# Performance work log

Hardware: AMD Instinct MI355X
Metric: run time of the kernel (lower is better)

The kernel has to match this reference:

```python
import jax, jax.numpy as jnp
import numpy as np

N, D, C = 8192, 512, 16
HM, HG = 256, 64  # mlp hidden, gcn hidden
ENHANCE = 6.0
LW0, LW1 = 1.0, 1.0  # loss_weight
NEG = jnp.float32(-9e15)


def setup_inputs() -> dict:
    key = jax.random.key(0)
    ks = jax.random.split(key, 12)
    feature = jax.random.normal(ks[0], (N, D), dtype=jnp.float32)
    # sparse symmetric binary adjacency with self loops (avg degree ~ 65)
    A = (jax.random.uniform(ks[1], (N, N)) < 0.004).astype(jnp.float32)
    adj = jnp.maximum(jnp.maximum(A, A.T), jnp.eye(N, dtype=jnp.float32))
    node_labels = jax.random.randint(ks[2], (N,), 0, C)
    labels_oneHot = jax.nn.one_hot(node_labels, C, dtype=jnp.float32)
    bias = jnp.ones((C, C), jnp.float32) + (ENHANCE - 1.0) * jnp.eye(C, dtype=jnp.float32)
    s = 0.05
    Wm1 = s * jax.random.normal(ks[3], (D, HM), dtype=jnp.float32)
    bm1 = jnp.zeros((HM,), jnp.float32)
    Wm2 = s * jax.random.normal(ks[4], (HM, C), dtype=jnp.float32)
    bm2 = jnp.zeros((C,), jnp.float32)
    W1 = s * jax.random.normal(ks[5], (D, HG), dtype=jnp.float32)
    b1 = jnp.zeros((HG,), jnp.float32)
    W2 = s * jax.random.normal(ks[6], (HG, C), dtype=jnp.float32)
    b2 = jnp.zeros((C,), jnp.float32)
    idx = jax.random.randint(ks[7], (1024,), 0, N)
    label = node_labels[idx]
    mask = jax.random.randint(ks[8], (N,), 0, 2).astype(bool)  # train mask
    return {"feature": feature, "adj": adj, "labels_oneHot": labels_oneHot,
            "bias": bias, "Wm1": Wm1, "bm1": bm1, "Wm2": Wm2, "bm2": bm2,
            "W1": W1, "b1": b1, "W2": W2, "b2": b2,
            "idx": idx, "label": label, "mask": mask}


def reference(feature, adj, labels_oneHot, bias, Wm1, bm1, Wm2, bm2,
              W1, b1, W2, b2, idx, label, mask):
    # MLP soft labels B: [N, C]
    B = jax.nn.softmax(jnp.maximum(feature @ Wm1 + bm1, 0.0) @ Wm2 + bm2, axis=1)
    # block matrix H: ground truth labels on train nodes, soft labels elsewhere
    soft_y = jnp.where(mask[:, None], labels_oneHot, B)          # [N, C]
    Hm = soft_y.T @ adj                                          # [C, N]
    H = (Hm @ soft_y) / jnp.sum(Hm, axis=1, keepdims=True)       # [C, C]
    Q = (H @ H.T) * bias
    Q = Q / jnp.sum(Q, axis=1, keepdims=True)                    # [C, C]
    # edge score B Q B^T, adjacency-masked softmax
    score = (B @ Q @ B.T) * adj                                  # [N, N]
    g = jax.nn.softmax(jnp.where(adj > 0, score, NEG), axis=1)   # [N, N]
    # 2-layer GCN with g as propagation matrix
    h = jnp.maximum(g @ (feature @ W1) + b1, 0.0)                # [N, HG]
    output = g @ (h @ W2) + b2                                   # [N, C]
    logits = jax.nn.softmax(output, axis=1)
    gcn_loss = -jnp.mean(jnp.log(logits[idx, label]))
    mlp_loss = -jnp.mean(jnp.log(B[idx, label]))
    final_loss = LW0 * gcn_loss + LW1 * mlp_loss
    return logits, final_loss, jax.lax.stop_gradient(H), jax.lax.stop_gradient(Q), jax.lax.stop_gradient(output)
```

## Files before the change

### kernel.cpp

```cpp
#include <hip/hip_runtime.h>
#include <math.h>

#define N   8192
#define D   512
#define C   16
#define HM  256
#define HG  64
#define KMAX 128

typedef __attribute__((ext_vector_type(8))) short bf16x8;
typedef __attribute__((ext_vector_type(4))) float f32x4;
typedef unsigned long long ull;

__device__ __forceinline__ unsigned short f2b(float x) {
  union { float f; unsigned int u; } v; v.f = x;
  unsigned int r = v.u + 0x7FFFu + ((v.u >> 16) & 1u);
  return (unsigned short)(r >> 16);
}
__device__ __forceinline__ float b2f(unsigned short b) {
  union { unsigned int u; float f; } v; v.u = ((unsigned int)b) << 16;
  return v.f;
}

__global__ __launch_bounds__(256) void tile_ballot(const float* __restrict__ adj,
    ull* __restrict__ bm, const float* __restrict__ Wm1, const float* __restrict__ W1,
    const float* __restrict__ Wm2, unsigned short* __restrict__ Wt,
    unsigned short* __restrict__ Wm2tb) {
  const int t = threadIdx.x;
  if (blockIdx.y == 64) {
    const int start = blockIdx.x * 256 + t;
    for (int i = start; i < 320 * 512; i += 129 * 256) {
      const int n = i >> 9, k = i & 511;
      Wt[i] = f2b((n < 256) ? Wm1[k * 256 + n] : W1[k * 64 + (n - 256)]);
    }
    for (int i = start; i < 16 * 256; i += 129 * 256) {
      const int cc = i >> 8, k = i & 255;
      Wm2tb[i] = f2b(Wm2[k * 16 + cc]);
    }
    return;
  }
  const int p = blockIdx.y;
  int I, J;
  if ((int)blockIdx.x < 128 - p) { I = p; J = p + blockIdx.x; }
  else                           { I = 127 - p; J = blockIdx.x - 1; }
  __shared__ unsigned char tb[64][68];
  #pragma unroll
  for (int rr = 0; rr < 4; ++rr) {
    const int r = rr * 16 + (t >> 4);
    const int c = (t & 15) * 4;
    const float4 v = *(const float4*)&adj[(size_t)(I * 64 + r) * N + J * 64 + c];
    tb[r][c + 0] = v.x > 0.f;
    tb[r][c + 1] = v.y > 0.f;
    tb[r][c + 2] = v.z > 0.f;
    tb[r][c + 3] = v.w > 0.f;
  }
  __syncthreads();
  const int lane = t & 63, w = t >> 6;
  #pragma unroll
  for (int i = 0; i < 16; ++i) {
    const int r = w * 16 + i;
    const ull rw = __ballot(tb[r][lane] != 0);
    if (lane == 0) bm[(size_t)(I * 64 + r) * 128 + J] = rw;
    const ull cw = __ballot(tb[lane][r] != 0);
    if (lane == 0) bm[(size_t)(J * 64 + r) * 128 + I] = cw;
  }
}

__global__ __launch_bounds__(256) void gemm_mlp(
    const float* __restrict__ feature, const bf16x8* __restrict__ Wt,
    const float* __restrict__ bm1, const bf16x8* __restrict__ Wm2tb,
    const float* __restrict__ bm2, const float* __restrict__ labels1h,
    const int* __restrict__ mask, float* __restrict__ Bmat,
    float* __restrict__ softy, unsigned short* __restrict__ X1b) {
  __shared__ unsigned short c1[32][264];
  const int l = threadIdx.x & 63, w = threadIdx.x >> 6;
  const int m0 = blockIdx.x * 32;
  const int kb = l >> 4, cl = l & 15;
  const int rw = (w >> 1) * 16;
  const int nt0 = (w & 1) * 10;
  const int row = m0 + rw + cl;
  const float* arow = feature + (size_t)row * D + kb * 8;
  f32x4 acc[10] = {};
  for (int kk = 0; kk < 16; ++kk) {
    const float4 a0 = *(const float4*)&arow[kk * 32];
    const float4 a1 = *(const float4*)&arow[kk * 32 + 4];
    bf16x8 af;
    af[0] = f2b(a0.x); af[1] = f2b(a0.y); af[2] = f2b(a0.z); af[3] = f2b(a0.w);
    af[4] = f2b(a1.x); af[5] = f2b(a1.y); af[6] = f2b(a1.z); af[7] = f2b(a1.w);
    #pragma unroll
    for (int i = 0; i < 10; ++i) {
      const bf16x8 bfr = Wt[(size_t)((nt0 + i) * 16 + cl) * 64 + kk * 4 + kb];
      acc[i] = __builtin_amdgcn_mfma_f32_16x16x32_bf16(af, bfr, acc[i], 0, 0, 0);
    }
  }
  const int rl0 = rw + kb * 4;
  #pragma unroll
  for (int i = 0; i < 10; ++i) {
    const int nt = nt0 + i;
    const int col = nt * 16 + cl;
    if (nt < 16) {
      const float bv = bm1[col];
      #pragma unroll
      for (int r = 0; r < 4; ++r)
        c1[rl0 + r][col] = f2b(fmaxf(acc[i][r] + bv, 0.f));
    } else {
      const int xc = col - 256;
      #pragma unroll
      for (int r = 0; r < 4; ++r)
        X1b[(size_t)(m0 + rl0 + r) * HG + xc] = f2b(acc[i][r]);
    }
  }
  __syncthreads();
  if ((w & 1) == 0) {
    f32x4 acc2 = {0.f, 0.f, 0.f, 0.f};
    #pragma unroll
    for (int kk = 0; kk < 8; ++kk) {
      const bf16x8 a2 = *(const bf16x8*)&c1[rw + cl][kk * 32 + kb * 8];
      const bf16x8 b2v = Wm2tb[(size_t)cl * 32 + kk * 4 + kb];
      acc2 = __builtin_amdgcn_mfma_f32_16x16x32_bf16(a2, b2v, acc2, 0, 0, 0);
    }
    const float bm2v = bm2[cl];
    #pragma unroll
    for (int r = 0; r < 4; ++r) {
      float v = acc2[r] + bm2v;
      float m = v;
      #pragma unroll
      for (int s = 1; s < 16; s <<= 1) m = fmaxf(m, __shfl_xor(m, s));
      const float e = __expf(v - m);
      float ssum = e;
      #pragma unroll
      for (int s = 1; s < 16; s <<= 1) ssum += __shfl_xor(ssum, s);
      const float bb = e / ssum;
      const int grow = m0 + rw + kb * 4 + r;
      Bmat[grow * C + cl] = bb;
      softy[grow * C + cl] = mask[grow] ? labels1h[grow * C + cl] : bb;
    }
  }
}

__global__ __launch_bounds__(256) void extract_nbr(const ull* __restrict__ bm,
    int* __restrict__ rowcnt, int* __restrict__ colidx,
    const float* __restrict__ softy, float* __restrict__ nbrsum) {
  __shared__ int cs[4][128];
  const int t = threadIdx.x, lane = t & 63, w = t >> 6;
  const int row = blockIdx.x * 4 + w;
  const ull w0 = bm[(size_t)row * 128 + lane];
  const ull w1 = bm[(size_t)row * 128 + 64 + lane];
  const int c0 = __builtin_popcountll(w0);
  const int c1 = __builtin_popcountll(w1);
  int s0 = c0, s1 = c1;
  #pragma unroll
  for (int s = 1; s < 64; s <<= 1) {
    const int y0 = __shfl_up(s0, s);
    const int y1 = __shfl_up(s1, s);
    if (lane >= s) { s0 += y0; s1 += y1; }
  }
  const int total0 = __shfl(s0, 63);
  const int total = total0 + __shfl(s1, 63);
  int off = s0 - c0;
  ull x = w0;
  while (x) {
    const int b = __builtin_ctzll(x);
    if (off < KMAX) {
      const int col = lane * 64 + b;
      colidx[(size_t)row * KMAX + off] = col;
      cs[w][off] = col;
    }
    ++off;
    x &= x - 1;
  }
  off = total0 + s1 - c1;
  x = w1;
  while (x) {
    const int b = __builtin_ctzll(x);
    if (off < KMAX) {
      const int col = (64 + lane) * 64 + b;
      colidx[(size_t)row * KMAX + off] = col;
      cs[w][off] = col;
    }
    ++off;
    x &= x - 1;
  }
  const int cnt = min(total, KMAX);
  if (lane == 0) rowcnt[row] = cnt;
  __syncthreads();
  const int cc = lane & 15, grp = lane >> 4;
  float acc = 0.f;
  for (int e = grp; e < cnt; e += 4)
    acc += softy[cs[w][e] * C + cc];
  acc += __shfl_xor(acc, 16);
  acc += __shfl_xor(acc, 32);
  if (lane < 16) nbrsum[row * C + cc] = acc;
}

__global__ __launch_bounds__(256) void h_partial(const float* __restrict__ nbrsum,
    const float* __restrict__ softy, float* __restrict__ Hpart) {
  const int t = threadIdx.x;
  const int c = t >> 4, cp = t & 15;
  float acc = 0.f, dacc = 0.f;
  const int j0 = blockIdx.x * (N / 64);
  for (int j = j0; j < j0 + N / 64; ++j) {
    const float nv = nbrsum[j * C + c];
    acc = fmaf(nv, softy[j * C + cp], acc);
    if (cp == 0) dacc += nv;
  }
  Hpart[blockIdx.x * 272 + t] = acc;
  if (cp == 0) Hpart[blockIdx.x * 272 + 256 + c] = dacc;
}

__global__ __launch_bounds__(256) void hq_final(const float* __restrict__ Hpart,
    const float* __restrict__ bias, float* __restrict__ H_out,
    float* __restrict__ Q_out, float* __restrict__ Qws) {
  __shared__ float Hs[256], Qs[256], rs[16], dd[16];
  const int t = threadIdx.x;
  const int c = t >> 4, cp = t & 15;
  float acc = 0.f;
  for (int b = 0; b < 64; ++b) acc += Hpart[b * 272 + t];
  if (t < 16) {
    float s = 0.f;
    for (int b = 0; b < 64; ++b) s += Hpart[b * 272 + 256 + t];
    dd[t] = s;
  }
  __syncthreads();
  const float Hv = acc / dd[c];
  Hs[t] = Hv;
  H_out[t] = Hv;
  __syncthreads();
  float q = 0.f;
  for (int k = 0; k < 16; ++k) q = fmaf(Hs[c * 16 + k], Hs[cp * 16 + k], q);
  q *= bias[t];
  Qs[t] = q;
  __syncthreads();
  if (t < 16) {
    float s = 0.f;
    for (int k = 0; k < 16; ++k) s += Qs[t * 16 + k];
    rs[t] = s;
  }
  __syncthreads();
  const float Qv = q / rs[c];
  Q_out[t] = Qv;
  Qws[t] = Qv;
}

__global__ __launch_bounds__(256) void edge_gcn1(const float* __restrict__ Bmat,
    const float* __restrict__ Q, const int* __restrict__ rowcnt,
    const int* __restrict__ colidx, const unsigned short* __restrict__ X1b,
    const float* __restrict__ b1, const float* __restrict__ W2,
    float* __restrict__ gval, float* __restrict__ X2) {
  __shared__ float Prow[4][16];
  __shared__ float gv[4][128];
  __shared__ int cs[4][128];
  const int lane = threadIdx.x & 63, w = threadIdx.x >> 6;
  const int row = blockIdx.x * 4 + w;
  const int c = lane & 15, grp = lane >> 4;
  float acc = 0.f;
  for (int k = grp * 4; k < grp * 4 + 4; ++k)
    acc = fmaf(Bmat[row * C + k], Q[k * C + c], acc);
  acc += __shfl_xor(acc, 16);
  acc += __shfl_xor(acc, 32);
  if (lane < 16) Prow[w][c] = acc;
  __syncthreads();
  const int cnt = rowcnt[row];
  const int col0 = (lane < cnt) ? colidx[row * KMAX + lane] : 0;
  const int col1 = (lane + 64 < cnt) ? colidx[row * KMAX + lane + 64] : 0;
  float s0 = -1e30f, s1 = -1e30f;
  if (lane < cnt) {
    float s = 0.f;
    for (int k = 0; k < 16; ++k) s = fmaf(Prow[w][k], Bmat[col0 * C + k], s);
    s0 = s;
  }
  if (lane + 64 < cnt) {
    float s = 0.f;
    for (int k = 0; k < 16; ++k) s = fmaf(Prow[w][k], Bmat[col1 * C + k], s);
    s1 = s;
  }
  float m = fmaxf(s0, s1);
  for (int s = 1; s < 64; s <<= 1) m = fmaxf(m, __shfl_xor(m, s));
  const float e0 = __expf(s0 - m), e1 = __expf(s1 - m);
  float ssum = e0 + e1;
  for (int s = 1; s < 64; s <<= 1) ssum += __shfl_xor(ssum, s);
  const float inv = 1.f / ssum;
  const float g0 = e0 * inv, g1 = e1 * inv;
  if (lane < cnt) gval[row * KMAX + lane] = g0;
  if (lane + 64 < cnt) gval[row * KMAX + lane + 64] = g1;
  gv[w][lane] = g0; gv[w][lane + 64] = g1;
  cs[w][lane] = col0; cs[w][lane + 64] = col1;
  __syncthreads();
  float hacc = 0.f;
  for (int e = 0; e < cnt; ++e)
    hacc = fmaf(gv[w][e], b2f(X1b[(size_t)cs[w][e] * HG + lane]), hacc);
  const float h = fmaxf(hacc + b1[lane], 0.f);
  float x[16];
  #pragma unroll
  for (int cc = 0; cc < 16; ++cc) x[cc] = h * W2[lane * C + cc];
  #pragma unroll
  for (int s = 1; s < 64; s <<= 1)
    #pragma unroll
    for (int cc = 0; cc < 16; ++cc) x[cc] += __shfl_xor(x[cc], s);
  float v = x[0];
  #pragma unroll
  for (int cc = 1; cc < 16; ++cc) v = (lane == cc) ? x[cc] : v;
  if (lane < 16) X2[row * C + lane] = v;
}

__global__ __launch_bounds__(256) void gcn2(const float* __restrict__ X2,
    const float* __restrict__ b2, const int* __restrict__ rowcnt,
    const int* __restrict__ colidx, const float* __restrict__ gval,
    float* __restrict__ out_logits, float* __restrict__ out_output) {
  const int lane = threadIdx.x & 63;
  const int row = blockIdx.x * 4 + (threadIdx.x >> 6);
  const int c = lane & 15, grp = lane >> 4;
  const int cnt = rowcnt[row];
  float acc = 0.f;
  for (int e = grp; e < cnt; e += 4)
    acc = fmaf(gval[row * KMAX + e], X2[colidx[row * KMAX + e] * C + c], acc);
  acc += __shfl_xor(acc, 16);
  acc += __shfl_xor(acc, 32);
  acc += b2[c];
  float m = acc;
  for (int s = 1; s < 16; s <<= 1) m = fmaxf(m, __shfl_xor(m, s));
  const float e = __expf(acc - m);
  float ssum = e;
  for (int s = 1; s < 16; s <<= 1) ssum += __shfl_xor(ssum, s);
  if (lane < 16) {
    out_output[row * C + c] = acc;
    out_logits[row * C + c] = e / ssum;
  }
}

__global__ __launch_bounds__(256) void loss_kernel(const float* __restrict__ logits,
    const float* __restrict__ Bmat, const int* __restrict__ idx,
    const int* __restrict__ label, float* __restrict__ out_loss) {
  __shared__ float sg[256], sm[256];
  const int t = threadIdx.x;
  float g = 0.f, m = 0.f;
  for (int i = t; i < 1024; i += 256) {
    const int ii = idx[i], ll = label[i];
    g -= logf(logits[ii * C + ll]);
    m -= logf(Bmat[ii * C + ll]);
  }
  sg[t] = g; sm[t] = m;
  __syncthreads();
  for (int s = 128; s > 0; s >>= 1) {
    if (t < s) { sg[t] += sg[t + s]; sm[t] += sm[t + s]; }
    __syncthreads();
  }
  if (t == 0) out_loss[0] = 1.0f * (sg[0] / 1024.f) + 1.0f * (sm[0] / 1024.f);
}

extern "C" void kernel_launch(void* const* d_in, const int* in_sizes, int n_in,
                              void* d_out, int out_size, void* d_ws, size_t ws_size,
                              hipStream_t stream) {
  const float* feature  = (const float*)d_in[0];
  const float* adj      = (const float*)d_in[1];
  const float* labels1h = (const float*)d_in[2];
  const float* bias     = (const float*)d_in[3];
  const float* Wm1 = (const float*)d_in[4];
  const float* bm1 = (const float*)d_in[5];
  const float* Wm2 = (const float*)d_in[6];
  const float* bm2 = (const float*)d_in[7];
  const float* W1  = (const float*)d_in[8];
  const float* b1  = (const float*)d_in[9];
  const float* W2  = (const float*)d_in[10];
  const float* b2  = (const float*)d_in[11];
  const int* idx   = (const int*)d_in[12];
  const int* label = (const int*)d_in[13];
  const int* mask  = (const int*)d_in[14];

  float* out = (float*)d_out;
  float* logits_o = out;
  float* loss_o   = out + (size_t)N * C;
  float* H_o      = loss_o + 1;
  float* Q_o      = H_o + 256;
  float* outp_o   = Q_o + 256;

  float* p = (float*)d_ws;
  float* Bmat   = p; p += (size_t)N * C;
  float* softy  = p; p += (size_t)N * C;
  float* nbrsum = p; p += (size_t)N * C;
  float* X2     = p; p += (size_t)N * C;
  float* Hpart  = p; p += 64 * 272;
  float* Qws    = p; p += 256;
  int* rowcnt = (int*)p; p += N;
  int* colidx = (int*)p; p += (size_t)N * KMAX;
  float* gval = p; p += (size_t)N * KMAX;
  unsigned short* X1b   = (unsigned short*)p; p += (size_t)N * HG / 2;
  unsigned short* Wt    = (unsigned short*)p; p += 320 * 512 / 2;
  unsigned short* Wm2tb = (unsigned short*)p; p += 16 * 256 / 2;
  ull* bm = (ull*)p;

  tile_ballot<<<dim3(129, 65), 256, 0, stream>>>(adj, bm, Wm1, W1, Wm2, Wt, Wm2tb);
  gemm_mlp<<<N / 32, 256, 0, stream>>>(feature, (const bf16x8*)Wt, bm1,
      (const bf16x8*)Wm2tb, bm2, labels1h, mask, Bmat, softy, X1b);
  extract_nbr<<<N / 4, 256, 0, stream>>>(bm, rowcnt, colidx, softy, nbrsum);
  h_partial<<<64, 256, 0, stream>>>(nbrsum, softy, Hpart);
  hq_final<<<1, 256, 0, stream>>>(Hpart, bias, H_o, Q_o, Qws);
  edge_gcn1<<<N / 4, 256, 0, stream>>>(Bmat, Qws, rowcnt, colidx, X1b, b1, W2, gval, X2);
  gcn2<<<N / 4, 256, 0, stream>>>(X2, b2, rowcnt, colidx, gval, logits_o, outp_o);
  loss_kernel<<<1, 256, 0, stream>>>(logits_o, Bmat, idx, label, loss_o);
}
```

Before: 126.9 us.

## Fuse adjacency ballot into MLP GEMM launch and split weight prep

Weight transposition and bf16 conversion move into a small separate kernel. The adjacency bitmask ballot and the MLP GEMM then run as two block ranges of one combined launch, so the bandwidth-bound adj scan overlaps with the compute-bound GEMM. Shared memory is reused through a union buffer. The GEMM blocks come first in the grid so they start early, at the cost of an extra launch for weight prep and a larger shared allocation for the ballot blocks.

```diff
diff --git a/kernel.cpp b/kernel.cpp
--- a/kernel.cpp
+++ b/kernel.cpp
@@ -22,58 +22,60 @@
   return v.f;
 }
 
-__global__ __launch_bounds__(256) void tile_ballot(const float* __restrict__ adj,
-    ull* __restrict__ bm, const float* __restrict__ Wm1, const float* __restrict__ W1,
-    const float* __restrict__ Wm2, unsigned short* __restrict__ Wt,
-    unsigned short* __restrict__ Wm2tb) {
+__global__ __launch_bounds__(256) void wprep(const float* __restrict__ Wm1,
+    const float* __restrict__ W1, const float* __restrict__ Wm2,
+    unsigned short* __restrict__ Wt, unsigned short* __restrict__ Wm2tb) {
+  const int tid = blockIdx.x * 256 + threadIdx.x;
+  {
+    const int n = tid >> 9, k = tid & 511;
+    Wt[tid] = f2b((n < 256) ? Wm1[k * 256 + n] : W1[k * 64 + (n - 256)]);
+  }
+  if (tid < 16 * 256) {
+    const int cc = tid >> 8, k = tid & 255;
+    Wm2tb[tid] = f2b(Wm2[k * 16 + cc]);
+  }
+}
+
+__global__ __launch_bounds__(256) void ballot_gemm(const float* __restrict__ adj,
+    ull* __restrict__ bm, const float* __restrict__ feature,
+    const bf16x8* __restrict__ Wt, const float* __restrict__ bm1,
+    const bf16x8* __restrict__ Wm2tb, const float* __restrict__ bm2,
+    const float* __restrict__ labels1h, const int* __restrict__ mask,
+    float* __restrict__ Bmat, float* __restrict__ softy,
+    unsigned short* __restrict__ X1b) {
+  __shared__ __align__(16) char smem[32 * 264 * 2];
   const int t = threadIdx.x;
-  if (blockIdx.y == 64) {
-    const int start = blockIdx.x * 256 + t;
-    for (int i = start; i < 320 * 512; i += 129 * 256) {
-      const int n = i >> 9, k = i & 511;
-      Wt[i] = f2b((n < 256) ? Wm1[k * 256 + n] : W1[k * 64 + (n - 256)]);
-    }
-    for (int i = start; i < 16 * 256; i += 129 * 256) {
-      const int cc = i >> 8, k = i & 255;
-      Wm2tb[i] = f2b(Wm2[k * 16 + cc]);
+  if (blockIdx.x >= 256) {
+    const int tri = blockIdx.x - 256;
+    const int p = tri / 129, q = tri % 129;
+    int I, J;
+    if (q < 128 - p) { I = p; J = p + q; }
+    else             { I = 127 - p; J = q - 1; }
+    unsigned char (*tb)[68] = (unsigned char(*)[68])smem;
+    #pragma unroll
+    for (int rr = 0; rr < 4; ++rr) {
+      const int r = rr * 16 + (t >> 4);
+      const int c = (t & 15) * 4;
+      const float4 v = *(const float4*)&adj[(size_t)(I * 64 + r) * N + J * 64 + c];
+      tb[r][c + 0] = v.x > 0.f;
+      tb[r][c + 1] = v.y > 0.f;
+      tb[r][c + 2] = v.z > 0.f;
+      tb[r][c + 3] = v.w > 0.f;
+    }
+    __syncthreads();
+    const int lane = t & 63, w = t >> 6;
+    #pragma unroll
+    for (int i = 0; i < 16; ++i) {
+      const int r = w * 16 + i;
+      const ull rw = __ballot(tb[r][lane] != 0);
+      if (lane == 0) bm[(size_t)(I * 64 + r) * 128 + J] = rw;
+      const ull cw = __ballot(tb[lane][r] != 0);
+      if (lane == 0) bm[(size_t)(J * 64 + r) * 128 + I] = cw;
     }
     return;
   }
-  const int p = blockIdx.y;
-  int I, J;
-  if ((int)blockIdx.x < 128 - p) { I = p; J = p + blockIdx.x; }
-  else                           { I = 127 - p; J = blockIdx.x - 1; }
-  __shared__ unsigned char tb[64][68];
-  #pragma unroll
-  for (int rr = 0; rr < 4; ++rr) {
-    const int r = rr * 16 + (t >> 4);
-    const int c = (t & 15) * 4;
-    const float4 v = *(const float4*)&adj[(size_t)(I * 64 + r) * N + J * 64 + c];
-    tb[r][c + 0] = v.x > 0.f;
-    tb[r][c + 1] = v.y > 0.f;
-    tb[r][c + 2] = v.z > 0.f;
-    tb[r][c + 3] = v.w > 0.f;
-  }
-  __syncthreads();
-  const int lane = t & 63, w = t >> 6;
-  #pragma unroll
-  for (int i = 0; i < 16; ++i) {
-    const int r = w * 16 + i;
-    const ull rw = __ballot(tb[r][lane] != 0);
-    if (lane == 0) bm[(size_t)(I * 64 + r) * 128 + J] = rw;
-    const ull cw = __ballot(tb[lane][r] != 0);
-    if (lane == 0) bm[(size_t)(J * 64 + r) * 128 + I] = cw;
-  }
-}
-
-__global__ __launch_bounds__(256) void gemm_mlp(
-    const float* __restrict__ feature, const bf16x8* __restrict__ Wt,
-    const float* __restrict__ bm1, const bf16x8* __restrict__ Wm2tb,
-    const float* __restrict__ bm2, const float* __restrict__ labels1h,
-    const int* __restrict__ mask, float* __restrict__ Bmat,
-    float* __restrict__ softy, unsigned short* __restrict__ X1b) {
-  __shared__ unsigned short c1[32][264];
-  const int l = threadIdx.x & 63, w = threadIdx.x >> 6;
+  unsigned short (*c1)[264] = (unsigned short(*)[264])smem;
+  const int l = t & 63, w = t >> 6;
   const int m0 = blockIdx.x * 32;
   const int kb = l >> 4, cl = l & 15;
   const int rw = (w >> 1) * 16;
@@ -389,9 +391,9 @@
   unsigned short* Wm2tb = (unsigned short*)p; p += 16 * 256 / 2;
   ull* bm = (ull*)p;
 
-  tile_ballot<<<dim3(129, 65), 256, 0, stream>>>(adj, bm, Wm1, W1, Wm2, Wt, Wm2tb);
-  gemm_mlp<<<N / 32, 256, 0, stream>>>(feature, (const bf16x8*)Wt, bm1,
-      (const bf16x8*)Wm2tb, bm2, labels1h, mask, Bmat, softy, X1b);
+  wprep<<<640, 256, 0, stream>>>(Wm1, W1, Wm2, Wt, Wm2tb);
+  ballot_gemm<<<256 + 8256, 256, 0, stream>>>(adj, bm, feature, (const bf16x8*)Wt,
+      bm1, (const bf16x8*)Wm2tb, bm2, labels1h, mask, Bmat, softy, X1b);
   extract_nbr<<<N / 4, 256, 0, stream>>>(bm, rowcnt, colidx, softy, nbrsum);
   h_partial<<<64, 256, 0, stream>>>(nbrsum, softy, Hpart);
   hq_final<<<1, 256, 0, stream>>>(Hpart, bias, H_o, Q_o, Qws);
```

After: 122.3 us, median of 2. 3.7% less time.
